# Performance work log

Measured on AMD Instinct MI355X. Metric: run time of the kernel, lower is better.

## Reference

```python
import jax, jax.numpy as jnp
import numpy as np

N, D_IN, D_OUT, H = 8192, 256, 128, 2
SLOPE = 0.2
EPS = 1e-5  # InstanceNorm2d default eps


def setup_inputs() -> dict:
    key = jax.random.key(0)
    ks = jax.random.split(key, 6)
    x = jax.random.normal(ks[0], (N, D_IN), dtype=jnp.float32)
    conn_mask = jnp.where(jax.random.uniform(ks[1], (N, N)) < 0.05, 0.0, -1e9).astype(jnp.float32)
    W = jax.random.normal(ks[2], (H, D_IN, D_OUT), dtype=jnp.float32) * 0.05
    a_src = jax.random.normal(ks[3], (H, D_OUT), dtype=jnp.float32) * 0.1
    a_tgt = jax.random.normal(ks[4], (H, D_OUT), dtype=jnp.float32) * 0.1
    W_res = jax.random.normal(ks[5], (D_OUT, D_IN), dtype=jnp.float32) * 0.05
    return {"x": x, "conn_mask": conn_mask, "W": W, "a_src": a_src, "a_tgt": a_tgt, "W_res": W_res}


def reference(x, conn_mask, W, a_src, a_tgt, W_res):
    # dropout is identity in eval mode
    proj = jnp.einsum('nd,hdf->hnf', x, W)                      # [H,N,F]
    s_src = jnp.einsum('hnf,hf->hn', proj, a_src)[:, :, None]   # [H,N,1]
    s_tgt = jnp.einsum('hnf,hf->hn', proj, a_tgt)[:, None, :]   # [H,1,N]
    scores = jax.nn.leaky_relu(s_src + s_tgt, negative_slope=SLOPE)  # [H,N,N]
    attn = jax.nn.softmax(conn_mask[None] + scores, axis=1)     # softmax over dim=1 as in torch code
    vals = jnp.einsum('hmn,hnf->hmf', attn, proj)               # bmm -> [H,N,F]
    vals = vals.mean(axis=0)                                    # head mean -> [N,F]
    # InstanceNorm2d(1, affine=False) over the whole [N,F] plane, biased variance
    mu = vals.mean()
    var = jnp.mean(jnp.square(vals - mu))
    vals_norm = (vals - mu) / jnp.sqrt(var + EPS)
    out = vals_norm + x @ W_res.T                               # residual projection (no bias)
    out = jax.nn.elu(out)
    return (out, conn_mask)
```

## Files before the change

kernel.cpp:

```cpp
#include <hip/hip_runtime.h>
#include <stdint.h>

#define NN   8192
#define DIN  256
#define FF   128
#define NF   (NN*FF)
#define SLOPE 0.2f
#define EPSI  1e-5f

typedef float vf4 __attribute__((ext_vector_type(4)));
typedef short bf16x8 __attribute__((ext_vector_type(8)));
typedef float f32x4 __attribute__((ext_vector_type(4)));

#define OFF_PROJ   0
#define OFF_RESID  (2*NF)
#define OFF_PACKED (3*NF)
#define OFF_SS     (4*NF)
#define OFF_ST     (OFF_SS + 2*NN)
#define OFF_CSUM   (OFF_ST + 2*NN)
#define OFF_STATS  (OFF_CSUM + 2*NN)
#define OFF_NTAB   (OFF_STATS + 16)
#define OFF_VALS   (OFF_NTAB + 4*NN)
#define OFF_WT     (OFF_VALS + NF)
#define OFF_PT2    (OFF_WT + DIN*FF)

__device__ __forceinline__ float lrelu(float x) { return x >= 0.f ? x : SLOPE * x; }

__device__ __forceinline__ uint32_t bfpack(float a, float b) {
  uint32_t ua = __float_as_uint(a); ua += 0x7fffu + ((ua >> 16) & 1u);
  uint32_t ub = __float_as_uint(b); ub += 0x7fffu + ((ub >> 16) & 1u);
  return (ua >> 16) | (ub & 0xffff0000u);
}

__global__ __launch_bounds__(256) void k_wt(const float* __restrict__ wres, float* __restrict__ wt) {
  int i = blockIdx.x * 256 + threadIdx.x;
  int d = i >> 7, f = i & 127;
  wt[i] = wres[f * DIN + d];
}

__global__ __launch_bounds__(256) void k_gemm(const float* __restrict__ x, const float* __restrict__ Wh,
                                              const float* __restrict__ wt, float* __restrict__ proj,
                                              float* __restrict__ resid) {
  const int h = blockIdx.y;
  const float* __restrict__ Wsrc = (h < 2) ? (Wh + h * (DIN * FF)) : wt;
  float* __restrict__ outp = (h < 2) ? (proj + h * NF) : resid;
  const int row0 = blockIdx.x * 64;
  __shared__ float xs[64 * 68];
  const int tid = threadIdx.x;
  const int ft = tid & 15, rt = tid >> 4;
  const int f0 = ft * 8, r0 = rt * 4;
  float acc[4][8];
#pragma unroll
  for (int j = 0; j < 4; ++j)
#pragma unroll
    for (int k = 0; k < 8; ++k) acc[j][k] = 0.f;

  for (int kc = 0; kc < 4; ++kc) {
    const int d0 = kc * 64;
#pragma unroll
    for (int k2 = 0; k2 < 4; ++k2) {
      int i = tid * 4 + k2 * 1024;
      int r = i >> 6, dd = i & 63;
      *(float4*)&xs[r * 68 + dd] = *(const float4*)&x[(row0 + r) * DIN + d0 + dd];
    }
    __syncthreads();
#pragma unroll
    for (int g = 0; g < 16; ++g) {
      const int dd = g * 4;
      float xr[4][4];
#pragma unroll
      for (int j = 0; j < 4; ++j) {
        float4 t = *(const float4*)&xs[(r0 + j) * 68 + dd];
        xr[j][0] = t.x; xr[j][1] = t.y; xr[j][2] = t.z; xr[j][3] = t.w;
      }
#pragma unroll
      for (int i = 0; i < 4; ++i) {
        float4 wa = *(const float4*)&Wsrc[(d0 + dd + i) * FF + f0];
        float4 wb = *(const float4*)&Wsrc[(d0 + dd + i) * FF + f0 + 4];
#pragma unroll
        for (int j = 0; j < 4; ++j) {
          float xx = xr[j][i];
          acc[j][0] += xx * wa.x; acc[j][1] += xx * wa.y; acc[j][2] += xx * wa.z; acc[j][3] += xx * wa.w;
          acc[j][4] += xx * wb.x; acc[j][5] += xx * wb.y; acc[j][6] += xx * wb.z; acc[j][7] += xx * wb.w;
        }
      }
    }
    __syncthreads();
  }
#pragma unroll
  for (int j = 0; j < 4; ++j) {
    int row = row0 + r0 + j;
    *(float4*)&outp[row * FF + f0]     = make_float4(acc[j][0], acc[j][1], acc[j][2], acc[j][3]);
    *(float4*)&outp[row * FF + f0 + 4] = make_float4(acc[j][4], acc[j][5], acc[j][6], acc[j][7]);
  }
}

__global__ __launch_bounds__(256) void k_sprep(const float* __restrict__ proj, const float* __restrict__ a_src,
                                               const float* __restrict__ a_tgt, float* __restrict__ ss,
                                               float* __restrict__ st, uint32_t* __restrict__ packed) {
  int lane = threadIdx.x & 63, wid = threadIdx.x >> 6;
  int n = blockIdx.x * 4 + wid;
  float2 q0 = *(const float2*)&proj[n * FF + 2 * lane];
  float2 q1 = *(const float2*)&proj[NF + n * FF + 2 * lane];
  float2 as0 = *(const float2*)&a_src[2 * lane];
  float2 at0 = *(const float2*)&a_tgt[2 * lane];
  float2 as1 = *(const float2*)&a_src[FF + 2 * lane];
  float2 at1 = *(const float2*)&a_tgt[FF + 2 * lane];
  float v0 = q0.x * as0.x + q0.y * as0.y;
  float v1 = q0.x * at0.x + q0.y * at0.y;
  float v2 = q1.x * as1.x + q1.y * as1.y;
  float v3 = q1.x * at1.x + q1.y * at1.y;
#pragma unroll
  for (int o = 1; o < 64; o <<= 1) {
    v0 += __shfl_xor(v0, o); v1 += __shfl_xor(v1, o);
    v2 += __shfl_xor(v2, o); v3 += __shfl_xor(v3, o);
  }
  uint2 pk;
  pk.x = bfpack(q0.x, q1.x);
  pk.y = bfpack(q0.y, q1.y);
  *(uint2*)&packed[n * FF + 2 * lane] = pk;
  if (lane == 0) { ss[n] = v0; ss[NN + n] = v2; st[n] = v1; st[NN + n] = v3; }
}

__global__ __launch_bounds__(256) void k_tpose(const uint32_t* __restrict__ packed, uint32_t* __restrict__ pt2) {
  __shared__ uint32_t sb[32][129];
  const int t = threadIdx.x, c = blockIdx.x;
  const int nl = t >> 3, fb = (t & 7) * 16;
#pragma unroll
  for (int i = 0; i < 4; ++i) {
    uint4 v = *(const uint4*)&packed[(c * 32 + nl) * FF + fb + i * 4];
    sb[nl][fb + i * 4] = v.x; sb[nl][fb + i * 4 + 1] = v.y;
    sb[nl][fb + i * 4 + 2] = v.z; sb[nl][fb + i * 4 + 3] = v.w;
  }
  __syncthreads();
  const int h = t >> 7, f = t & 127;
  uint32_t wbuf[16];
#pragma unroll
  for (int p = 0; p < 16; ++p) {
    uint32_t a = sb[2 * p][f], b = sb[2 * p + 1][f];
    wbuf[p] = h ? ((a >> 16) | (b & 0xffff0000u)) : ((a & 0xffffu) | (b << 16));
  }
  uint32_t* dst = pt2 + ((c * 2 + h) * 128 + f) * 16;
#pragma unroll
  for (int i = 0; i < 4; ++i)
    *(uint4*)&dst[i * 4] = make_uint4(wbuf[i * 4], wbuf[i * 4 + 1], wbuf[i * 4 + 2], wbuf[i * 4 + 3]);
}

__global__ __launch_bounds__(256) void k_scan(const float* __restrict__ mask, float* __restrict__ maskout,
                                              const float* __restrict__ ss, const float* __restrict__ st,
                                              float* __restrict__ csum, uint32_t* __restrict__ bitmask) {
  const int tid = threadIdx.x;
  const int lane = tid & 63, wv = tid >> 6;
  const int n = blockIdx.x * 256 + tid;
  const int m0 = blockIdx.y * 128;
  const int wbase = blockIdx.x * 8 + wv * 2;
  const float st0 = st[n], st1 = st[NN + n];
  const float ssA = ss[m0 + lane],      ssB = ss[m0 + 64 + lane];
  const float ssC = ss[NN + m0 + lane], ssD = ss[NN + m0 + 64 + lane];
  float c0 = 0.f, c1 = 0.f;

  for (int i = 0; i < 128; i += 8) {
    float v[8];
#pragma unroll
    for (int r = 0; r < 8; ++r)
      v[r] = __builtin_nontemporal_load(&mask[(size_t)(m0 + i + r) * NN + n]);
#pragma unroll
    for (int r = 0; r < 8; ++r) {
      const int m = m0 + i + r;
      __builtin_nontemporal_store(v[r], &maskout[(size_t)m * NN + n]);
      bool e = v[r] > -0.5e9f;
      unsigned long long bm = __ballot(e);
      if (lane == 0)
        *(uint2*)&bitmask[m * 256 + wbase] = make_uint2((uint32_t)bm, (uint32_t)(bm >> 32));
      const int ri = i + r;
      float s0 = __uint_as_float(__builtin_amdgcn_readlane(
                   __float_as_uint(ri < 64 ? ssA : ssB), ri & 63));
      float s1 = __uint_as_float(__builtin_amdgcn_readlane(
                   __float_as_uint(ri < 64 ? ssC : ssD), ri & 63));
      float w0 = __expf(lrelu(s0 + st0));
      float w1 = __expf(lrelu(s1 + st1));
      c0 += e ? w0 : 0.f;
      c1 += e ? w1 : 0.f;
    }
  }
  atomicAdd(&csum[n], c0);
  atomicAdd(&csum[NN + n], c1);
}

__global__ __launch_bounds__(256) void k_ntab(const float* __restrict__ st, const float* __restrict__ csum,
                                              float4* __restrict__ ntab) {
  int i = blockIdx.x * 256 + threadIdx.x;
  ntab[i] = make_float4(st[i], st[NN + i], 1.f / csum[i], 1.f / csum[NN + i]);
}

__global__ __launch_bounds__(128) void k_vals(const uint32_t* __restrict__ bitmask, const uint32_t* __restrict__ pt2,
                                              const float4* __restrict__ ntab, const float* __restrict__ ss,
                                              float* __restrict__ vals, float* __restrict__ stats) {
  __shared__ short lds_B[2][128][40];
  __shared__ short lds_A[2][32][40];
  const int t = threadIdx.x;
  const int lane = t & 63, wid = t >> 6;
  const int m0 = blockIdx.x * 32;
  const int q = lane >> 4, col = lane & 15;
  const int n2 = t & 15, mg = t >> 4;

  float ssm0[4], ssm1[4];
#pragma unroll
  for (int p = 0; p < 4; ++p) {
    ssm0[p] = ss[m0 + mg + 8 * p];
    ssm1[p] = ss[NN + m0 + mg + 8 * p];
  }

  f32x4 acc[8];
#pragma unroll
  for (int i = 0; i < 8; ++i) acc[i] = (f32x4){0.f, 0.f, 0.f, 0.f};

  uint32_t* ldsb_w = (uint32_t*)&lds_B[0][0][0];

  for (int step = 0; step < NN / 32; ++step) {
    const int n0 = step * 32;
    const uint32_t* src = pt2 + step * 4096;
#pragma unroll
    for (int i = 0; i < 8; ++i) {
      uint4 v = *(const uint4*)&src[t * 4 + i * 512];
      int row = (t >> 2) + i * 32, c4 = (t & 3) * 4;
      *(uint4*)&ldsb_w[row * 20 + c4] = v;
    }
    float4 na = ntab[n0 + 2 * n2];
    float4 nb = ntab[n0 + 2 * n2 + 1];
#pragma unroll
    for (int p = 0; p < 4; ++p) {
      const int ml = mg + 8 * p;
      uint32_t bw = bitmask[(size_t)(m0 + ml) * 256 + (n0 >> 5)];
      float e0a = __expf(lrelu(ssm0[p] + na.x)) * na.z;
      float e1a = __expf(lrelu(ssm1[p] + na.y)) * na.w;
      float e0b = __expf(lrelu(ssm0[p] + nb.x)) * nb.z;
      float e1b = __expf(lrelu(ssm1[p] + nb.y)) * nb.w;
      bool b0 = (bw >> (2 * n2)) & 1, b1 = (bw >> (2 * n2 + 1)) & 1;
      e0a = b0 ? e0a : 0.f; e1a = b0 ? e1a : 0.f;
      e0b = b1 ? e0b : 0.f; e1b = b1 ? e1b : 0.f;
      *(uint32_t*)&lds_A[0][ml][2 * n2] = bfpack(e0a, e0b);
      *(uint32_t*)&lds_A[1][ml][2 * n2] = bfpack(e1a, e1b);
    }
    __syncthreads();
    bf16x8 a0 = *(const bf16x8*)&lds_A[0][wid * 16 + col][q * 8];
    bf16x8 a1 = *(const bf16x8*)&lds_A[1][wid * 16 + col][q * 8];
#pragma unroll
    for (int ft = 0; ft < 8; ++ft) {
      bf16x8 b0 = *(const bf16x8*)&lds_B[0][ft * 16 + col][q * 8];
      acc[ft] = __builtin_amdgcn_mfma_f32_16x16x32_bf16(a0, b0, acc[ft], 0, 0, 0);
      bf16x8 b1 = *(const bf16x8*)&lds_B[1][ft * 16 + col][q * 8];
      acc[ft] = __builtin_amdgcn_mfma_f32_16x16x32_bf16(a1, b1, acc[ft], 0, 0, 0);
    }
    __syncthreads();
  }

  float s = 0.f, qq = 0.f;
#pragma unroll
  for (int ft = 0; ft < 8; ++ft) {
#pragma unroll
    for (int r = 0; r < 4; ++r) {
      int mrow = m0 + wid * 16 + q * 4 + r;
      float v = 0.5f * acc[ft][r];
      vals[mrow * FF + ft * 16 + col] = v;
      s += v; qq += v * v;
    }
  }
#pragma unroll
  for (int o = 1; o < 64; o <<= 1) { s += __shfl_xor(s, o); qq += __shfl_xor(qq, o); }
  if (lane == 0) { atomicAdd(stats, s); atomicAdd(stats + 1, qq); }
}

__global__ __launch_bounds__(256) void k_final(const float* __restrict__ vals, const float* __restrict__ resid,
                                               const float* __restrict__ stats, float* __restrict__ out) {
  int i = (blockIdx.x * 256 + threadIdx.x) * 4;
  float mu = stats[0] * (1.f / NF);
  float var = stats[1] * (1.f / NF) - mu * mu;
  float rs = rsqrtf(var + EPSI);
  float4 v = *(const float4*)&vals[i];
  float4 r = *(const float4*)&resid[i];
  float t0 = (v.x - mu) * rs + r.x;
  float t1 = (v.y - mu) * rs + r.y;
  float t2 = (v.z - mu) * rs + r.z;
  float t3 = (v.w - mu) * rs + r.w;
  float4 o;
  o.x = t0 > 0.f ? t0 : expm1f(t0);
  o.y = t1 > 0.f ? t1 : expm1f(t1);
  o.z = t2 > 0.f ? t2 : expm1f(t2);
  o.w = t3 > 0.f ? t3 : expm1f(t3);
  *(float4*)&out[i] = o;
}

extern "C" void kernel_launch(void* const* d_in, const int* in_sizes, int n_in,
                              void* d_out, int out_size, void* d_ws, size_t ws_size,
                              hipStream_t stream) {
  const float* x     = (const float*)d_in[0];
  const float* mask  = (const float*)d_in[1];
  const float* W     = (const float*)d_in[2];
  const float* a_src = (const float*)d_in[3];
  const float* a_tgt = (const float*)d_in[4];
  const float* wres  = (const float*)d_in[5];
  float* out = (float*)d_out;
  float* wsf = (float*)d_ws;

  float*    proj    = wsf + OFF_PROJ;
  uint32_t* bitmask = (uint32_t*)(wsf + OFF_PROJ);
  float*    resid   = wsf + OFF_RESID;
  uint32_t* packed  = (uint32_t*)(wsf + OFF_PACKED);
  float*    ss      = wsf + OFF_SS;
  float*    st      = wsf + OFF_ST;
  float*    csum    = wsf + OFF_CSUM;
  float*    stats   = wsf + OFF_STATS;
  float4*   ntab    = (float4*)(wsf + OFF_NTAB);
  float*    vals    = wsf + OFF_VALS;
  float*    wt      = wsf + OFF_WT;
  uint32_t* pt2     = (uint32_t*)(wsf + OFF_PT2);

  (void)hipMemsetAsync(csum, 0, (2 * NN + 16) * sizeof(float), stream);

  hipLaunchKernelGGL(k_wt,    dim3(DIN * FF / 256), dim3(256), 0, stream, wres, wt);
  hipLaunchKernelGGL(k_gemm,  dim3(NN / 64, 3),     dim3(256), 0, stream, x, W, wt, proj, resid);
  hipLaunchKernelGGL(k_sprep, dim3(NN / 4),         dim3(256), 0, stream, proj, a_src, a_tgt, ss, st, packed);
  hipLaunchKernelGGL(k_tpose, dim3(NN / 32),        dim3(256), 0, stream, packed, pt2);
  hipLaunchKernelGGL(k_scan,  dim3(NN / 256, NN / 128), dim3(256), 0, stream, mask, out + NF, ss, st, csum, bitmask);
  hipLaunchKernelGGL(k_ntab,  dim3(NN / 256),       dim3(256), 0, stream, st, csum, ntab);
  hipLaunchKernelGGL(k_vals,  dim3(NN / 32),        dim3(128), 0, stream, bitmask, pt2, ntab, ss, vals, stats);
  hipLaunchKernelGGL(k_final, dim3(NF / 1024),      dim3(256), 0, stream, vals, resid, stats, out);
}
```

Measured before the change: 840.0 us.

## Split k_vals reduction over 8 N-chunks with atomic accumulation and fragment-ordered LDS

The attention-times-projection kernel is split along the reduction dimension into 8 chunks via a second grid dimension, so there are 8x more blocks (2048 instead of 256) to fill the GPU. Partial results are accumulated into a pre-zeroed vals buffer with float atomics. The mean/variance statistics move to a separate k_stats pass. The LDS tiles are also re-laid out in MFMA fragment order. The cost is an extra memset, an extra kernel, many global atomics, and a reduction order that is no longer deterministic.

```diff
diff --git a/kernel.cpp b/kernel.cpp
--- a/kernel.cpp
+++ b/kernel.cpp
@@ -195,14 +195,16 @@
 
 __global__ __launch_bounds__(128) void k_vals(const uint32_t* __restrict__ bitmask, const uint32_t* __restrict__ pt2,
                                               const float4* __restrict__ ntab, const float* __restrict__ ss,
-                                              float* __restrict__ vals, float* __restrict__ stats) {
-  __shared__ short lds_B[2][128][40];
-  __shared__ short lds_A[2][32][40];
+                                              float* __restrict__ vals) {
+  __shared__ short B2[2][8][4][16][8];
+  __shared__ short A2[2][2][4][16][8];
   const int t = threadIdx.x;
   const int lane = t & 63, wid = t >> 6;
   const int m0 = blockIdx.x * 32;
+  const int nc = blockIdx.y;
   const int q = lane >> 4, col = lane & 15;
   const int n2 = t & 15, mg = t >> 4;
+  const int tft = t >> 4, tcol = t & 15;
 
   float ssm0[4], ssm1[4];
 #pragma unroll
@@ -215,22 +217,27 @@
 #pragma unroll
   for (int i = 0; i < 8; ++i) acc[i] = (f32x4){0.f, 0.f, 0.f, 0.f};
 
-  uint32_t* ldsb_w = (uint32_t*)&lds_B[0][0][0];
-
-  for (int step = 0; step < NN / 32; ++step) {
-    const int n0 = step * 32;
-    const uint32_t* src = pt2 + step * 4096;
-#pragma unroll
-    for (int i = 0; i < 8; ++i) {
-      uint4 v = *(const uint4*)&src[t * 4 + i * 512];
-      int row = (t >> 2) + i * 32, c4 = (t & 3) * 4;
-      *(uint4*)&ldsb_w[row * 20 + c4] = v;
+  uint32_t* B2w = (uint32_t*)&B2[0][0][0][0][0];
+  uint32_t* A2w = (uint32_t*)&A2[0][0][0][0][0];
+
+  for (int s = 0; s < 32; ++s) {
+    const int n0 = nc * 1024 + s * 32;
+    const uint32_t* src = pt2 + (n0 >> 5) * 4096;
+#pragma unroll
+    for (int h = 0; h < 2; ++h) {
+      const uint4* p4 = (const uint4*)&src[(h * 128 + t) * 16];
+#pragma unroll
+      for (int k = 0; k < 4; ++k) {
+        uint4 v = p4[k];
+        *(uint4*)&B2w[(((h * 8 + tft) * 4 + k) * 16 + tcol) * 4] = v;
+      }
     }
     float4 na = ntab[n0 + 2 * n2];
     float4 nb = ntab[n0 + 2 * n2 + 1];
 #pragma unroll
     for (int p = 0; p < 4; ++p) {
       const int ml = mg + 8 * p;
+      const int mt = ml >> 4, mcol = ml & 15;
       uint32_t bw = bitmask[(size_t)(m0 + ml) * 256 + (n0 >> 5)];
       float e0a = __expf(lrelu(ssm0[p] + na.x)) * na.z;
       float e1a = __expf(lrelu(ssm1[p] + na.y)) * na.w;
@@ -239,36 +246,41 @@
       bool b0 = (bw >> (2 * n2)) & 1, b1 = (bw >> (2 * n2 + 1)) & 1;
       e0a = b0 ? e0a : 0.f; e1a = b0 ? e1a : 0.f;
       e0b = b1 ? e0b : 0.f; e1b = b1 ? e1b : 0.f;
-      *(uint32_t*)&lds_A[0][ml][2 * n2] = bfpack(e0a, e0b);
-      *(uint32_t*)&lds_A[1][ml][2 * n2] = bfpack(e1a, e1b);
+      int base = ((0 * 2 + mt) * 4 + (n2 >> 2)) * 64 + mcol * 4 + (n2 & 3);
+      A2w[base] = bfpack(e0a, e0b);
+      A2w[base + 2 * 4 * 64] = bfpack(e1a, e1b);
     }
     __syncthreads();
-    bf16x8 a0 = *(const bf16x8*)&lds_A[0][wid * 16 + col][q * 8];
-    bf16x8 a1 = *(const bf16x8*)&lds_A[1][wid * 16 + col][q * 8];
+    bf16x8 a0 = *(const bf16x8*)&A2[0][wid][q][col][0];
+    bf16x8 a1 = *(const bf16x8*)&A2[1][wid][q][col][0];
 #pragma unroll
     for (int ft = 0; ft < 8; ++ft) {
-      bf16x8 b0 = *(const bf16x8*)&lds_B[0][ft * 16 + col][q * 8];
+      bf16x8 b0 = *(const bf16x8*)&B2[0][ft][q][col][0];
       acc[ft] = __builtin_amdgcn_mfma_f32_16x16x32_bf16(a0, b0, acc[ft], 0, 0, 0);
-      bf16x8 b1 = *(const bf16x8*)&lds_B[1][ft * 16 + col][q * 8];
+      bf16x8 b1 = *(const bf16x8*)&B2[1][ft][q][col][0];
       acc[ft] = __builtin_amdgcn_mfma_f32_16x16x32_bf16(a1, b1, acc[ft], 0, 0, 0);
     }
     __syncthreads();
   }
 
-  float s = 0.f, qq = 0.f;
 #pragma unroll
   for (int ft = 0; ft < 8; ++ft) {
 #pragma unroll
     for (int r = 0; r < 4; ++r) {
       int mrow = m0 + wid * 16 + q * 4 + r;
-      float v = 0.5f * acc[ft][r];
-      vals[mrow * FF + ft * 16 + col] = v;
-      s += v; qq += v * v;
-    }
-  }
-#pragma unroll
-  for (int o = 1; o < 64; o <<= 1) { s += __shfl_xor(s, o); qq += __shfl_xor(qq, o); }
-  if (lane == 0) { atomicAdd(stats, s); atomicAdd(stats + 1, qq); }
+      atomicAdd(&vals[mrow * FF + ft * 16 + col], 0.5f * acc[ft][r]);
+    }
+  }
+}
+
+__global__ __launch_bounds__(256) void k_stats(const float* __restrict__ vals, float* __restrict__ stats) {
+  int i = blockIdx.x * 256 + threadIdx.x;
+  float4 v = *(const float4*)&vals[i * 4];
+  float s = v.x + v.y + v.z + v.w;
+  float q = v.x * v.x + v.y * v.y + v.z * v.z + v.w * v.w;
+#pragma unroll
+  for (int o = 1; o < 64; o <<= 1) { s += __shfl_xor(s, o); q += __shfl_xor(q, o); }
+  if ((threadIdx.x & 63) == 0) { atomicAdd(stats, s); atomicAdd(stats + 1, q); }
 }
 
 __global__ __launch_bounds__(256) void k_final(const float* __restrict__ vals, const float* __restrict__ resid,
@@ -317,6 +329,7 @@
   uint32_t* pt2     = (uint32_t*)(wsf + OFF_PT2);
 
   (void)hipMemsetAsync(csum, 0, (2 * NN + 16) * sizeof(float), stream);
+  (void)hipMemsetAsync(vals, 0, NF * sizeof(float), stream);
 
   hipLaunchKernelGGL(k_wt,    dim3(DIN * FF / 256), dim3(256), 0, stream, wres, wt);
   hipLaunchKernelGGL(k_gemm,  dim3(NN / 64, 3),     dim3(256), 0, stream, x, W, wt, proj, resid);
@@ -324,6 +337,7 @@
   hipLaunchKernelGGL(k_tpose, dim3(NN / 32),        dim3(256), 0, stream, packed, pt2);
   hipLaunchKernelGGL(k_scan,  dim3(NN / 256, NN / 128), dim3(256), 0, stream, mask, out + NF, ss, st, csum, bitmask);
   hipLaunchKernelGGL(k_ntab,  dim3(NN / 256),       dim3(256), 0, stream, st, csum, ntab);
-  hipLaunchKernelGGL(k_vals,  dim3(NN / 32),        dim3(128), 0, stream, bitmask, pt2, ntab, ss, vals, stats);
+  hipLaunchKernelGGL(k_vals,  dim3(NN / 32, 8),     dim3(128), 0, stream, bitmask, pt2, ntab, ss, vals);
+  hipLaunchKernelGGL(k_stats, dim3(NF / 1024),      dim3(256), 0, stream, vals, stats);
   hipLaunchKernelGGL(k_final, dim3(NF / 1024),      dim3(256), 0, stream, vals, resid, stats, out);
 }
```

After: 732.5 us. 1.15x faster.
